# Kernel tuning notes

Measured on AMD Instinct MI355X. Metric: run time of the kernel, lower is better.

Reference implementation:

```python
import jax, jax.numpy as jnp
import numpy as np

INPUT, HIDDEN, LAYERS = 512, 1024, 2
BATCH, SEQ = 64, 512


def _gru_layer(x, h0, W_ih, W_hh, b_ih, b_hh):
    """Run one GRU layer over time. x: [B,T,D_in], h0: [B,H] -> (out [B,T,H], h_T [B,H])."""
    H = h0.shape[-1]
    # Input-side gates are time-independent: precompute as one big GEMM.
    gi = jnp.einsum('btd,gd->btg', x, W_ih) + b_ih  # [B,T,3H]

    def step(h, gi_t):
        gh = h @ W_hh.T + b_hh                      # [B,3H]
        i_r, i_z, i_n = jnp.split(gi_t, 3, axis=1)
        h_r, h_z, h_n = jnp.split(gh, 3, axis=1)
        r = jax.nn.sigmoid(i_r + h_r)
        z = jax.nn.sigmoid(i_z + h_z)
        n = jnp.tanh(i_n + r * h_n)
        h_new = (1 - z) * h + z * n
        return h_new, h_new

    h_T, out = jax.lax.scan(step, h0, jnp.swapaxes(gi, 0, 1))  # scan over time
    return jnp.swapaxes(out, 0, 1), h_T


def setup_inputs() -> dict:
    key = jax.random.key(0)
    ks = jax.random.split(key, 8)
    stdv = 1.0 / np.sqrt(HIDDEN)

    def u(k, shape):
        return jax.random.uniform(k, shape, jnp.float32, -stdv, stdv)

    return {
        'x': jax.random.normal(ks[0], (BATCH, SEQ, INPUT), jnp.float32),
        'h0': jnp.zeros((LAYERS, BATCH, HIDDEN), jnp.float32),
        'W_ih0': u(ks[1], (3 * HIDDEN, INPUT)),
        'W_hh0': u(ks[2], (3 * HIDDEN, HIDDEN)),
        'b_ih0': jnp.zeros((3 * HIDDEN,), jnp.float32),
        'b_hh0': jnp.zeros((3 * HIDDEN,), jnp.float32),
        'W_ih1': u(ks[3], (3 * HIDDEN, HIDDEN)),
        'W_hh1': u(ks[4], (3 * HIDDEN, HIDDEN)),
        'b_ih1': jnp.zeros((3 * HIDDEN,), jnp.float32),
        'b_hh1': jnp.zeros((3 * HIDDEN,), jnp.float32),
    }


def reference(x, h0, W_ih0, W_hh0, b_ih0, b_hh0, W_ih1, W_hh1, b_ih1, b_hh1):
    # Layer-by-layer is mathematically identical to the per-timestep interleaved
    # loop in the torch code (layer l at time t depends only on layer l-1 up to t).
    out0, hT0 = _gru_layer(x, h0[0], W_ih0, W_hh0, b_ih0, b_hh0)
    out1, hT1 = _gru_layer(out0, h0[1], W_ih1, W_hh1, b_ih1, b_hh1)
    h_n = jnp.stack([hT0, hT1])  # [num_layers, B, H]
    return out1, h_n
```

## Files before the change

kernel.cpp:

```cpp
#include <hip/hip_runtime.h>
#include <math.h>

#define HID  1024
#define SEQ  512
#define NB   64
#define DIN0 512

using short8 = __attribute__((ext_vector_type(8))) short;
using f32x4  = __attribute__((ext_vector_type(4))) float;

__device__ __forceinline__ unsigned short f2bf(float f) {
    unsigned int u = __float_as_uint(f);
    u += 0x7fffu + ((u >> 16) & 1u);
    return (unsigned short)(u >> 16);
}
__device__ __forceinline__ float sigm_(float x) { return 1.0f / (1.0f + __expf(-x)); }
__device__ __forceinline__ float tanh_(float x) {
    float ax = fabsf(x);
    float e = __expf(-2.0f * ax);
    float t = (1.0f - e) / (1.0f + e);
    return copysignf(t, x);
}

__device__ __forceinline__ void ld_coh(short8* a, const unsigned short* p) {
    asm volatile("global_load_dwordx4 %0, %1, off sc0 sc1" : "=&v"(*a) : "v"(p) : "memory");
}
__device__ __forceinline__ void ld_pln(short8* a, const unsigned short* p) {
    asm volatile("global_load_dwordx4 %0, %1, off" : "=&v"(*a) : "v"(p) : "memory");
}
__device__ __forceinline__ void st_coh_u16(unsigned short* p, unsigned short v) {
    asm volatile("global_store_short %0, %1, off sc0 sc1" :: "v"(p), "v"((unsigned)v) : "memory");
}

template<int LAYER>
__device__ __forceinline__ void gru_loop(
    const unsigned short* __restrict__ xb,
    const unsigned short* __restrict__ Wi, const unsigned short* __restrict__ Wh,
    const float* __restrict__ bi, const float* __restrict__ bh_,
    float* __restrict__ hf, unsigned short* __restrict__ hb,
    float* __restrict__ out, unsigned* __restrict__ bar,
    int bid, float (*lds)[2][4][272])
{
    constexpr int Din = LAYER ? HID : DIN0;
    constexpr int K   = Din + HID;
    constexpr int Kq  = K / 8;
    constexpr int NK  = Kq / 32;

    const int q   = bid & 127;
    const int j0  = (q >> 1) << 4;
    const int b0  = (q & 1) << 5;
    const int tid = threadIdx.x;
    const int l   = tid & 63;
    const int w   = tid >> 6;
    const int c   = l & 15;
    const int kg  = l >> 4;
    const int kq0 = w * Kq;

    short8 Br[NK], Bz[NK], Bn[NK];
#pragma unroll
    for (int s = 0; s < NK; ++s) {
        const int k0 = kq0 + s * 32 + kg * 8;
        const unsigned short *pr, *pz, *pn;
        if (k0 < Din) {
            pr = Wi + (long)(j0 + c) * Din + k0;
            pz = Wi + (long)(HID + j0 + c) * Din + k0;
            pn = Wi + (long)(2 * HID + j0 + c) * Din + k0;
        } else {
            pr = Wh + (long)(j0 + c) * HID + (k0 - Din);
            pz = Wh + (long)(HID + j0 + c) * HID + (k0 - Din);
            pn = Wh + (long)(2 * HID + j0 + c) * HID + (k0 - Din);
        }
        Br[s] = *(const short8*)pr;
        Bz[s] = *(const short8*)pz;
        Bn[s] = *(const short8*)pn;
    }

    const long hrow0 = (long)(b0 + c) * HID;
    const long hrow1 = (long)(b0 + 16 + c) * HID;
    const long xrow0 = (long)(b0 + c) * SEQ * DIN0;
    const long xrow1 = (long)(b0 + 16 + c) * SEQ * DIN0;

    const int cb  = tid >> 4;
    const int jc  = tid & 15;
    const int cm  = cb >> 4, cbr = cb & 15;
    const int j   = j0 + jc;
    const float bir = bi[j], biz = bi[HID + j], bin = bi[2 * HID + j];
    const float bhr = bh_[j], bhz = bh_[HID + j], bhn = bh_[2 * HID + j];

    for (int i = 0; i <= SEQ; ++i) {
        const int st = LAYER ? (i - 1) : i;
        if (st >= 0 && st < SEQ) {
            const int rp = st & 1, wp = rp ^ 1;
            const unsigned short* Alo = hb + (long)(0 * 2 + wp) * NB * HID;
            const unsigned short* Ahi = hb + (long)(LAYER * 2 + rp) * NB * HID;
            const unsigned short* xp0 = xb + xrow0 + (long)st * DIN0;
            const unsigned short* xp1 = xb + xrow1 + (long)st * DIN0;

            f32x4 acc_r[2], acc_z[2], acc_nx[2], acc_nh[2];
#pragma unroll
            for (int m = 0; m < 2; ++m) {
                acc_r[m] = (f32x4){0.f, 0.f, 0.f, 0.f};
                acc_z[m] = (f32x4){0.f, 0.f, 0.f, 0.f};
                acc_nx[m] = (f32x4){0.f, 0.f, 0.f, 0.f};
                acc_nh[m] = (f32x4){0.f, 0.f, 0.f, 0.f};
            }

            short8 abuf[4][2];

#define ISSUE(g) do {                                                          \
    const int kk_ = kq0 + (g) * 32 + kg * 8;                                   \
    const bool lo_ = (kq0 + (g) * 32) < Din;                                   \
    if (LAYER == 0) {                                                          \
        if (lo_) { ld_pln(&abuf[(g) & 3][0], xp0 + kk_);                       \
                   ld_pln(&abuf[(g) & 3][1], xp1 + kk_); }                     \
        else     { ld_coh(&abuf[(g) & 3][0], Ahi + hrow0 + (kk_ - Din));       \
                   ld_coh(&abuf[(g) & 3][1], Ahi + hrow1 + (kk_ - Din)); }     \
    } else {                                                                   \
        const unsigned short* bse_ = lo_ ? (Alo + kk_) : (Ahi + (kk_ - HID));  \
        ld_coh(&abuf[(g) & 3][0], bse_ + hrow0);                               \
        ld_coh(&abuf[(g) & 3][1], bse_ + hrow1);                               \
    } } while (0)

#define MSTEP(s) do {                                                                                  \
    const bool lo_ = (kq0 + (s) * 32) < Din;                                                           \
    acc_r[0] = __builtin_amdgcn_mfma_f32_16x16x32_bf16(abuf[(s) & 3][0], Br[s], acc_r[0], 0, 0, 0);    \
    acc_r[1] = __builtin_amdgcn_mfma_f32_16x16x32_bf16(abuf[(s) & 3][1], Br[s], acc_r[1], 0, 0, 0);    \
    acc_z[0] = __builtin_amdgcn_mfma_f32_16x16x32_bf16(abuf[(s) & 3][0], Bz[s], acc_z[0], 0, 0, 0);    \
    acc_z[1] = __builtin_amdgcn_mfma_f32_16x16x32_bf16(abuf[(s) & 3][1], Bz[s], acc_z[1], 0, 0, 0);    \
    if (lo_) {                                                                                         \
        acc_nx[0] = __builtin_amdgcn_mfma_f32_16x16x32_bf16(abuf[(s) & 3][0], Bn[s], acc_nx[0], 0, 0, 0); \
        acc_nx[1] = __builtin_amdgcn_mfma_f32_16x16x32_bf16(abuf[(s) & 3][1], Bn[s], acc_nx[1], 0, 0, 0); \
    } else {                                                                                           \
        acc_nh[0] = __builtin_amdgcn_mfma_f32_16x16x32_bf16(abuf[(s) & 3][0], Bn[s], acc_nh[0], 0, 0, 0); \
        acc_nh[1] = __builtin_amdgcn_mfma_f32_16x16x32_bf16(abuf[(s) & 3][1], Bn[s], acc_nh[1], 0, 0, 0); \
    } } while (0)

#define KSTEP(s, W) do {                                                       \
    if ((s) + 3 < NK) ISSUE((s) + 3);                                          \
    asm volatile("s_waitcnt vmcnt(" #W ")" ::: "memory");                      \
    __builtin_amdgcn_sched_barrier(0);                                         \
    MSTEP(s); } while (0)

            ISSUE(0); ISSUE(1); ISSUE(2);
            if constexpr (NK == 8) {
                KSTEP(0, 6); KSTEP(1, 6); KSTEP(2, 6); KSTEP(3, 6);
                KSTEP(4, 6); KSTEP(5, 4); KSTEP(6, 2); KSTEP(7, 0);
            } else {
                KSTEP(0, 6); KSTEP(1, 6); KSTEP(2, 6);
                KSTEP(3, 4); KSTEP(4, 2); KSTEP(5, 0);
            }
#undef ISSUE
#undef MSTEP
#undef KSTEP

            if (w >= 4) {
#pragma unroll
                for (int m = 0; m < 2; ++m)
#pragma unroll
                    for (int v = 0; v < 4; ++v) {
                        const int rc = (kg * 4 + v) * 17 + c;
                        lds[w - 4][m][0][rc] = acc_r[m][v];
                        lds[w - 4][m][1][rc] = acc_z[m][v];
                        lds[w - 4][m][2][rc] = acc_nx[m][v];
                        lds[w - 4][m][3][rc] = acc_nh[m][v];
                    }
            }
            __syncthreads();
            if (w < 4) {
#pragma unroll
                for (int m = 0; m < 2; ++m)
#pragma unroll
                    for (int v = 0; v < 4; ++v) {
                        const int rc = (kg * 4 + v) * 17 + c;
                        lds[w][m][0][rc] += acc_r[m][v];
                        lds[w][m][1][rc] += acc_z[m][v];
                        lds[w][m][2][rc] += acc_nx[m][v];
                        lds[w][m][3][rc] += acc_nh[m][v];
                    }
            }
            __syncthreads();

            float rr = 0.f, zz = 0.f, nx = 0.f, nh = 0.f;
#pragma unroll
            for (int ww = 0; ww < 4; ++ww) {
                rr += lds[ww][cm][0][cbr * 17 + jc];
                zz += lds[ww][cm][1][cbr * 17 + jc];
                nx += lds[ww][cm][2][cbr * 17 + jc];
                nh += lds[ww][cm][3][cbr * 17 + jc];
            }
            const float r = sigm_(rr + bir + bhr);
            const float z = sigm_(zz + biz + bhz);
            const float n = tanh_((nx + bin) + r * (nh + bhn));
            const int bgl = b0 + cb;
            const long pofs = ((long)(LAYER * 2 + rp) * NB + bgl) * HID + j;
            const long nofs = ((long)(LAYER * 2 + wp) * NB + bgl) * HID + j;
            const float hp = hf[pofs];
            const float hnew = (1.f - z) * hp + z * n;
            hf[nofs] = hnew;
            st_coh_u16(hb + nofs, f2bf(hnew));
            if (LAYER) out[((long)bgl * SEQ + st) * HID + j] = hnew;
        }

        asm volatile("s_waitcnt vmcnt(0)" ::: "memory");
        __syncthreads();
        if (tid == 0) {
            unsigned* gen = bar + (bid & 7) * 16;
            unsigned* sub = bar + 160 + (bid & 7) * 16;
            unsigned g = __hip_atomic_load(gen, __ATOMIC_RELAXED, __HIP_MEMORY_SCOPE_AGENT);
            if (__hip_atomic_fetch_add(sub, 1u, __ATOMIC_RELAXED, __HIP_MEMORY_SCOPE_AGENT) == 31u) {
                __hip_atomic_store(sub, 0u, __ATOMIC_RELAXED, __HIP_MEMORY_SCOPE_AGENT);
                asm volatile("s_waitcnt vmcnt(0)" ::: "memory");
                unsigned* root = bar + 128;
                if (__hip_atomic_fetch_add(root, 1u, __ATOMIC_RELAXED, __HIP_MEMORY_SCOPE_AGENT) == 7u) {
                    __hip_atomic_store(root, 0u, __ATOMIC_RELAXED, __HIP_MEMORY_SCOPE_AGENT);
                    asm volatile("s_waitcnt vmcnt(0)" ::: "memory");
#pragma unroll
                    for (int gg = 0; gg < 8; ++gg)
                        __hip_atomic_fetch_add(bar + gg * 16, 1u, __ATOMIC_RELAXED, __HIP_MEMORY_SCOPE_AGENT);
                }
            }
            while (__hip_atomic_load(gen, __ATOMIC_RELAXED, __HIP_MEMORY_SCOPE_AGENT) == g)
                __builtin_amdgcn_s_sleep(2);
        }
        __syncthreads();
    }
}

__global__ __launch_bounds__(512, 2) void gru_persist(
    const unsigned short* __restrict__ xb,
    const unsigned short* __restrict__ W0i, const unsigned short* __restrict__ W0h,
    const unsigned short* __restrict__ W1i, const unsigned short* __restrict__ W1h,
    const float* __restrict__ bi0, const float* __restrict__ bh0,
    const float* __restrict__ bi1, const float* __restrict__ bh1,
    float* __restrict__ hf, unsigned short* __restrict__ hb,
    float* __restrict__ out, unsigned* __restrict__ bar)
{
    __shared__ float lds[4][2][4][272];
    const int bid = blockIdx.x;
    if (bid < 128) gru_loop<0>(xb, W0i, W0h, bi0, bh0, hf, hb, out, bar, bid, lds);
    else           gru_loop<1>(xb, W1i, W1h, bi1, bh1, hf, hb, out, bar, bid, lds);
}

__global__ __launch_bounds__(256) void cvt_bf16(const float* __restrict__ src,
                                                unsigned short* __restrict__ dst, int n4) {
    int i = blockIdx.x * 256 + threadIdx.x;
    if (i >= n4) return;
    float4 f = *(const float4*)(src + 4L * i);
    unsigned long long u =  (unsigned long long)f2bf(f.x)
                         | ((unsigned long long)f2bf(f.y) << 16)
                         | ((unsigned long long)f2bf(f.z) << 32)
                         | ((unsigned long long)f2bf(f.w) << 48);
    *(unsigned long long*)(dst + 4L * i) = u;
}

__global__ __launch_bounds__(256) void init_h(const float* __restrict__ h0,
                                              float* __restrict__ hf,
                                              unsigned short* __restrict__ hb) {
    int i = blockIdx.x * 256 + threadIdx.x;
    int layer = i >> 16, idx = i & 65535;
    float v = h0[i];
    hf[(long)(layer * 2 + 0) * 65536 + idx] = v;
    hb[(long)(layer * 2 + 0) * 65536 + idx] = f2bf(v);
}

extern "C" void kernel_launch(void* const* d_in, const int* in_sizes, int n_in,
                              void* d_out, int out_size, void* d_ws, size_t ws_size,
                              hipStream_t stream) {
    const float* x    = (const float*)d_in[0];
    const float* h0   = (const float*)d_in[1];
    const float* Wih0 = (const float*)d_in[2];
    const float* Whh0 = (const float*)d_in[3];
    const float* bih0 = (const float*)d_in[4];
    const float* bhh0 = (const float*)d_in[5];
    const float* Wih1 = (const float*)d_in[6];
    const float* Whh1 = (const float*)d_in[7];
    const float* bih1 = (const float*)d_in[8];
    const float* bhh1 = (const float*)d_in[9];

    float* out   = (float*)d_out;
    float* hnout = out + (long)NB * SEQ * HID;

    unsigned short* W0i = (unsigned short*)d_ws;
    unsigned short* W0h = W0i + 3072L * 512;
    unsigned short* W1i = W0h + 3072L * 1024;
    unsigned short* W1h = W1i + 3072L * 1024;
    float*          hf  = (float*)(W1h + 3072L * 1024);
    unsigned short* hb  = (unsigned short*)(hf + 4L * 65536);
    unsigned*       bar = (unsigned*)(hb + 4L * 65536);
    unsigned short* xb  = (unsigned short*)(bar + 512);

    hipMemsetAsync(bar, 0, 2048, stream);

    cvt_bf16<<<(3072 * 512 / 4  + 255) / 256, 256, 0, stream>>>(Wih0, W0i, 3072 * 512 / 4);
    cvt_bf16<<<(3072 * 1024 / 4 + 255) / 256, 256, 0, stream>>>(Whh0, W0h, 3072 * 1024 / 4);
    cvt_bf16<<<(3072 * 1024 / 4 + 255) / 256, 256, 0, stream>>>(Wih1, W1i, 3072 * 1024 / 4);
    cvt_bf16<<<(3072 * 1024 / 4 + 255) / 256, 256, 0, stream>>>(Whh1, W1h, 3072 * 1024 / 4);
    cvt_bf16<<<(NB * SEQ * DIN0 / 4 + 255) / 256, 256, 0, stream>>>(x, xb, NB * SEQ * DIN0 / 4);
    init_h<<<512, 256, 0, stream>>>(h0, hf, hb);

    gru_persist<<<256, 512, 0, stream>>>(xb, W0i, W0h, W1i, W1h,
                                         bih0, bhh0, bih1, bhh1,
                                         hf, hb, out, bar);

    hipMemcpyAsync(hnout,         hf,              65536 * sizeof(float),
                   hipMemcpyDeviceToDevice, stream);
    hipMemcpyAsync(hnout + 65536, hf + 2L * 65536, 65536 * sizeof(float),
                   hipMemcpyDeviceToDevice, stream);
}
```

Before: 3.975 ms.

## Replace tree grid barrier with flag-based barrier and single-pass LDS reduction

The two-level atomic counter barrier becomes a flag barrier: each block writes its step number to a per-block flag, block 0 polls all 256 flags with one wavefront and then bumps 8 generation counters that the other blocks spin on. The cross-wave reduction now has all 8 waves write packed float4 partials to LDS in one pass, removing one __syncthreads and the read-modify-write step. The barrier is also skipped after the final timestep. The costs are a larger LDS footprint, which may matter at 2 blocks per CU, and block 0 serialising the barrier release.

Result: faster. 3.288 ms, median of 2 (-17.3%).

```diff
diff --git a/kernel.cpp b/kernel.cpp
--- a/kernel.cpp
+++ b/kernel.cpp
@@ -39,7 +39,7 @@
     const float* __restrict__ bi, const float* __restrict__ bh_,
     float* __restrict__ hf, unsigned short* __restrict__ hb,
     float* __restrict__ out, unsigned* __restrict__ bar,
-    int bid, float (*lds)[2][4][272])
+    int bid, float (*lds)[2][16][68])
 {
     constexpr int Din = LAYER ? HID : DIN0;
     constexpr int K   = Din + HID;
@@ -55,6 +55,9 @@
     const int c   = l & 15;
     const int kg  = l >> 4;
     const int kq0 = w * Kq;
+
+    unsigned* gens  = bar;
+    unsigned* flags = bar + 128;
 
     short8 Br[NK], Bz[NK], Bn[NK];
 #pragma unroll
@@ -153,40 +156,20 @@
 #undef MSTEP
 #undef KSTEP
 
-            if (w >= 4) {
-#pragma unroll
-                for (int m = 0; m < 2; ++m)
-#pragma unroll
-                    for (int v = 0; v < 4; ++v) {
-                        const int rc = (kg * 4 + v) * 17 + c;
-                        lds[w - 4][m][0][rc] = acc_r[m][v];
-                        lds[w - 4][m][1][rc] = acc_z[m][v];
-                        lds[w - 4][m][2][rc] = acc_nx[m][v];
-                        lds[w - 4][m][3][rc] = acc_nh[m][v];
-                    }
-            }
+#pragma unroll
+            for (int m = 0; m < 2; ++m)
+#pragma unroll
+                for (int v = 0; v < 4; ++v) {
+                    f32x4 pk = { acc_r[m][v], acc_z[m][v], acc_nx[m][v], acc_nh[m][v] };
+                    *(f32x4*)&lds[w][m][kg * 4 + v][c * 4] = pk;
+                }
             __syncthreads();
-            if (w < 4) {
-#pragma unroll
-                for (int m = 0; m < 2; ++m)
-#pragma unroll
-                    for (int v = 0; v < 4; ++v) {
-                        const int rc = (kg * 4 + v) * 17 + c;
-                        lds[w][m][0][rc] += acc_r[m][v];
-                        lds[w][m][1][rc] += acc_z[m][v];
-                        lds[w][m][2][rc] += acc_nx[m][v];
-                        lds[w][m][3][rc] += acc_nh[m][v];
-                    }
-            }
-            __syncthreads();
 
             float rr = 0.f, zz = 0.f, nx = 0.f, nh = 0.f;
 #pragma unroll
-            for (int ww = 0; ww < 4; ++ww) {
-                rr += lds[ww][cm][0][cbr * 17 + jc];
-                zz += lds[ww][cm][1][cbr * 17 + jc];
-                nx += lds[ww][cm][2][cbr * 17 + jc];
-                nh += lds[ww][cm][3][cbr * 17 + jc];
+            for (int ww = 0; ww < 8; ++ww) {
+                f32x4 g = *(const f32x4*)&lds[ww][cm][cbr][jc * 4];
+                rr += g[0]; zz += g[1]; nx += g[2]; nh += g[3];
             }
             const float r = sigm_(rr + bir + bhr);
             const float z = sigm_(zz + biz + bhz);
@@ -201,28 +184,34 @@
             if (LAYER) out[((long)bgl * SEQ + st) * HID + j] = hnew;
         }
 
+        if (i == SEQ) break;
+
         asm volatile("s_waitcnt vmcnt(0)" ::: "memory");
         __syncthreads();
-        if (tid == 0) {
-            unsigned* gen = bar + (bid & 7) * 16;
-            unsigned* sub = bar + 160 + (bid & 7) * 16;
-            unsigned g = __hip_atomic_load(gen, __ATOMIC_RELAXED, __HIP_MEMORY_SCOPE_AGENT);
-            if (__hip_atomic_fetch_add(sub, 1u, __ATOMIC_RELAXED, __HIP_MEMORY_SCOPE_AGENT) == 31u) {
-                __hip_atomic_store(sub, 0u, __ATOMIC_RELAXED, __HIP_MEMORY_SCOPE_AGENT);
-                asm volatile("s_waitcnt vmcnt(0)" ::: "memory");
-                unsigned* root = bar + 128;
-                if (__hip_atomic_fetch_add(root, 1u, __ATOMIC_RELAXED, __HIP_MEMORY_SCOPE_AGENT) == 7u) {
-                    __hip_atomic_store(root, 0u, __ATOMIC_RELAXED, __HIP_MEMORY_SCOPE_AGENT);
-                    asm volatile("s_waitcnt vmcnt(0)" ::: "memory");
-#pragma unroll
-                    for (int gg = 0; gg < 8; ++gg)
-                        __hip_atomic_fetch_add(bar + gg * 16, 1u, __ATOMIC_RELAXED, __HIP_MEMORY_SCOPE_AGENT);
-                }
-            }
-            while (__hip_atomic_load(gen, __ATOMIC_RELAXED, __HIP_MEMORY_SCOPE_AGENT) == g)
-                __builtin_amdgcn_s_sleep(2);
+        const unsigned tgt = (unsigned)(i + 1);
+        if (tid == 0)
+            __hip_atomic_store(flags + bid, tgt, __ATOMIC_RELAXED, __HIP_MEMORY_SCOPE_AGENT);
+        if (bid == 0) {
+            if (tid < 64) {
+                bool ok;
+                do {
+                    unsigned f0 = __hip_atomic_load(flags + tid,       __ATOMIC_RELAXED, __HIP_MEMORY_SCOPE_AGENT);
+                    unsigned f1 = __hip_atomic_load(flags + 64 + tid,  __ATOMIC_RELAXED, __HIP_MEMORY_SCOPE_AGENT);
+                    unsigned f2 = __hip_atomic_load(flags + 128 + tid, __ATOMIC_RELAXED, __HIP_MEMORY_SCOPE_AGENT);
+                    unsigned f3 = __hip_atomic_load(flags + 192 + tid, __ATOMIC_RELAXED, __HIP_MEMORY_SCOPE_AGENT);
+                    ok = (f0 >= tgt) & (f1 >= tgt) & (f2 >= tgt) & (f3 >= tgt);
+                } while (!__all(ok));
+                if (tid < 8)
+                    __hip_atomic_store(gens + tid * 16, tgt, __ATOMIC_RELAXED, __HIP_MEMORY_SCOPE_AGENT);
+            }
+            __syncthreads();
+        } else {
+            if (tid == 0) {
+                while (__hip_atomic_load(gens + (bid & 7) * 16, __ATOMIC_RELAXED, __HIP_MEMORY_SCOPE_AGENT) < tgt)
+                    __builtin_amdgcn_s_sleep(2);
+            }
+            __syncthreads();
         }
-        __syncthreads();
     }
 }
 
@@ -235,7 +224,7 @@
     float* __restrict__ hf, unsigned short* __restrict__ hb,
     float* __restrict__ out, unsigned* __restrict__ bar)
 {
-    __shared__ float lds[4][2][4][272];
+    __shared__ float lds[8][2][16][68];
     const int bid = blockIdx.x;
     if (bid < 128) gru_loop<0>(xb, W0i, W0h, bi0, bh0, hf, hb, out, bar, bid, lds);
     else           gru_loop<1>(xb, W1i, W1h, bi1, bh1, hf, hb, out, bar, bid, lds);
```
